# Kernel tuning notes

Hardware: AMD Instinct MI355X
Metric: run time of the kernel (lower is better)

## Reference

```python
import jax, jax.numpy as jnp
import numpy as np

TOP_K = 2
SCALE = 1.0  # score_scale_factor

def setup_inputs() -> dict:
    key = jax.random.key(0)
    ks = jax.random.split(key, 8)
    T, D, E, F = 4096, 1024, 8, 4096
    return {
        "hidden_states": jax.random.normal(ks[0], (T, D), jnp.float32),
        "gw1": jax.random.normal(ks[1], (D, D // 4), jnp.float32) * 0.02,
        "gb1": jnp.zeros((D // 4,), jnp.float32),
        "gw2": jax.random.normal(ks[2], (D // 4, D // 16), jnp.float32) * 0.02,
        "gb2": jnp.zeros((D // 16,), jnp.float32),
        "gw3": jax.random.normal(ks[3], (D // 16, E), jnp.float32) * 0.02,
        "w1": jax.random.normal(ks[4], (E, D, F), jnp.float32) * 0.02,
        "b1": jnp.zeros((E, F), jnp.float32),
        "w2": jax.random.normal(ks[5], (E, F, D), jnp.float32) * 0.02,
        "b2": jnp.zeros((E, D), jnp.float32),
    }

def reference(hidden_states, gw1, gb1, gw2, gb2, gw3, w1, b1, w2, b2):
    h = hidden_states                              # [T, D]
    g = jax.nn.relu(h @ gw1 + gb1)
    g = jax.nn.relu(g @ gw2 + gb2)
    router_logits = g @ gw3                        # [T, E]
    probs = jax.nn.softmax(router_logits.astype(jnp.float32), axis=-1)
    top_w, top_i = jax.lax.top_k(probs, TOP_K)     # [T, k]
    top_w = top_w / jnp.sum(top_w, axis=-1, keepdims=True)
    top_w = top_w.astype(h.dtype)
    T, E = router_logits.shape
    # combine weights: scatter normalized top-k weights into dense [T, E]
    cw = jnp.zeros((T, E), h.dtype).at[jnp.arange(T)[:, None], top_i].add(top_w)
    out = jnp.zeros_like(h)
    for e in range(E):  # small fixed expert count
        y = jax.nn.gelu(h @ w1[e] + b1[e]) @ w2[e] + b2[e]
        out = out + y * (cw[:, e:e + 1] * SCALE)
    return out, router_logits
```

## Files before the change

### kernel.cpp

```cpp
#include <hip/hip_runtime.h>
#include <stdint.h>

#define T_  4096
#define D_  1024
#define E_  8
#define F_  4096
#define H1_ 256
#define H2_ 64
#define SCALE_ 1.0f
#define NROW_ (2 * T_)
#define NT2_ 40

typedef unsigned short ushort_t;
typedef unsigned int   uint32;
typedef __attribute__((ext_vector_type(8))) short  short8;
typedef __attribute__((ext_vector_type(4))) float  f32x4;
typedef __attribute__((ext_vector_type(8))) unsigned short us8;

#define BARRIER() do { asm volatile("" ::: "memory"); __builtin_amdgcn_s_barrier(); asm volatile("" ::: "memory"); } while (0)
#define WAITVM(N) asm volatile("s_waitcnt vmcnt(" #N ")" ::: "memory")

__device__ __forceinline__ ushort_t f2bf(float f) {
  uint32 u = __float_as_uint(f);
  u += 0x7FFFu + ((u >> 16) & 1u);
  return (ushort_t)(u >> 16);
}
__device__ __forceinline__ float gelu_tanh(float x) {
  float u = 0.7978845608028654f * (x + 0.044715f * x * x * x);
  float e = __expf(2.0f * u);
  return 0.5f * x * (1.0f + (1.0f - 2.0f / (e + 1.0f)));
}
__device__ __forceinline__ void gll16(const void* gptr, void* lptr) {
  void* g = const_cast<void*>(gptr);
  __builtin_amdgcn_global_load_lds((__attribute__((address_space(1))) void*)g,
                                   (__attribute__((address_space(3))) void*)lptr,
                                   16, 0, 0);
}

__device__ __forceinline__ void stage8(const ushort_t* a0, const ushort_t* a1,
                                       const ushort_t* b0, const ushort_t* b1,
                                       short8 (*An)[16][64], short8 (*Bn)[16][64], int w) {
  gll16(a0,      &An[0][w * 2 + 0][0]);
  gll16(a0 + 32, &An[1][w * 2 + 0][0]);
  gll16(a1,      &An[0][w * 2 + 1][0]);
  gll16(a1 + 32, &An[1][w * 2 + 1][0]);
  gll16(b0,      &Bn[0][w * 2 + 0][0]);
  gll16(b0 + 32, &Bn[1][w * 2 + 0][0]);
  gll16(b1,      &Bn[0][w * 2 + 1][0]);
  gll16(b1 + 32, &Bn[1][w * 2 + 1][0]);
}

__device__ __forceinline__ void mfma_step64(const short8 (*Ac)[16][64], const short8 (*Bc)[16][64],
                                            int wr, int wc, int lane, f32x4 acc[8][4]) {
#pragma unroll
  for (int ks = 0; ks < 2; ++ks) {
    short8 af[8], bf4[4];
#pragma unroll
    for (int i = 0; i < 8; ++i) af[i] = Ac[ks][wr * 8 + i][lane];
#pragma unroll
    for (int j = 0; j < 4; ++j) bf4[j] = Bc[ks][wc * 4 + j][lane];
#pragma unroll
    for (int i = 0; i < 8; ++i)
#pragma unroll
      for (int j = 0; j < 4; ++j)
        acc[i][j] = __builtin_amdgcn_mfma_f32_16x16x32_bf16(af[i], bf4[j], acc[i][j], 0, 0, 0);
  }
}

__global__ void k_cvt_h(const float* __restrict__ h, ushort_t* __restrict__ hb) {
  int i = (blockIdx.x * 256 + threadIdx.x) * 8;
  float4 a = *(const float4*)(h + i);
  float4 b = *(const float4*)(h + i + 4);
  short8 v;
  v[0] = (short)f2bf(a.x); v[1] = (short)f2bf(a.y);
  v[2] = (short)f2bf(a.z); v[3] = (short)f2bf(a.w);
  v[4] = (short)f2bf(b.x); v[5] = (short)f2bf(b.y);
  v[6] = (short)f2bf(b.z); v[7] = (short)f2bf(b.w);
  *(short8*)(hb + i) = v;
}

__global__ void k_transpose_bf16(const float* __restrict__ in, ushort_t* __restrict__ out,
                                 int R, int C) {
  __shared__ float ltf[64][65];
  const size_t per = (size_t)R * C;
  const float* src = in + per * blockIdx.z;
  ushort_t* dst = out + per * blockIdx.z;
  int r0 = blockIdx.x * 64, c0 = blockIdx.y * 64;
  int tid = threadIdx.x;
  int cg = (tid & 15) * 4;
  int rr = tid >> 4;
#pragma unroll
  for (int rb = 0; rb < 64; rb += 16) {
    int r = rb + rr;
    float4 v = *(const float4*)(src + (size_t)(r0 + r) * C + c0 + cg);
    ltf[r][cg + 0] = v.x; ltf[r][cg + 1] = v.y;
    ltf[r][cg + 2] = v.z; ltf[r][cg + 3] = v.w;
  }
  __syncthreads();
  int c = tid >> 2, rch = (tid & 3) * 16;
  ushort_t tmp[16];
#pragma unroll
  for (int i = 0; i < 16; ++i) tmp[i] = f2bf(ltf[rch + i][c]);
  ushort_t* dp = dst + (size_t)(c0 + c) * R + r0 + rch;
  *(us8*)dp = *(const us8*)&tmp[0];
  *(us8*)(dp + 8) = *(const us8*)&tmp[8];
}

__global__ void k_router1(const float* __restrict__ h, const float* __restrict__ gw1,
                          double* __restrict__ p1) {
  __shared__ float sA[16][65];
  __shared__ float sB[16][65];
  int tx = threadIdx.x, ty = threadIdx.y;
  int tid = ty * 16 + tx;
  int m0 = blockIdx.y * 64, n0 = blockIdx.x * 64;
  int kc = blockIdx.z;
  double acc[4][4] = {};
  for (int k0 = kc * 256; k0 < kc * 256 + 256; k0 += 16) {
    {
      int m = tid & 63, kq = tid >> 6;
      float4 v = *(const float4*)(h + (size_t)(m0 + m) * D_ + k0 + kq * 4);
      sA[kq*4+0][m] = v.x; sA[kq*4+1][m] = v.y; sA[kq*4+2][m] = v.z; sA[kq*4+3][m] = v.w;
    }
    {
      int k = tid >> 4, nq = tid & 15;
      float4 v = *(const float4*)(gw1 + (size_t)(k0 + k) * H1_ + n0 + nq * 4);
      sB[k][nq*4+0] = v.x; sB[k][nq*4+1] = v.y; sB[k][nq*4+2] = v.z; sB[k][nq*4+3] = v.w;
    }
    __syncthreads();
#pragma unroll
    for (int k = 0; k < 16; ++k) {
      float a[4], b[4];
#pragma unroll
      for (int i = 0; i < 4; ++i) a[i] = sA[k][ty + i * 16];
#pragma unroll
      for (int j = 0; j < 4; ++j) b[j] = sB[k][tx * 4 + j];
#pragma unroll
      for (int i = 0; i < 4; ++i)
#pragma unroll
        for (int j = 0; j < 4; ++j)
          acc[i][j] += (double)a[i] * (double)b[j];
    }
    __syncthreads();
  }
  double* pd = p1 + (size_t)kc * T_ * H1_;
  for (int i = 0; i < 4; ++i)
    for (int j = 0; j < 4; ++j) {
      int m = m0 + ty + i * 16, n = n0 + tx * 4 + j;
      pd[(size_t)m * H1_ + n] = acc[i][j];
    }
}

__global__ void k_router23(const double* __restrict__ p1, const float* __restrict__ gb1,
                           const float* __restrict__ gw2, const float* __restrict__ gb2,
                           const float* __restrict__ gw3,
                           float* __restrict__ logits_out, int* __restrict__ tokExp,
                           float* __restrict__ tokW, int* __restrict__ counts) {
  __shared__ double sG1[4][256];
  __shared__ double sG2[4][64];
  __shared__ double sL[4][8];
  int lane = threadIdx.x & 63, wv = threadIdx.x >> 6;
  int t = blockIdx.x * 4 + wv;
  const size_t TH = (size_t)T_ * H1_;
  const double* gp = p1 + (size_t)t * H1_ + lane * 4;
  double s0 = 0, s1 = 0, s2 = 0, s3 = 0;
#pragma unroll
  for (int kc = 0; kc < 4; ++kc) {
    double2 va = *(const double2*)(gp + kc * TH);
    double2 vb = *(const double2*)(gp + kc * TH + 2);
    s0 += va.x; s1 += va.y; s2 += vb.x; s3 += vb.y;
  }
  int hbase = lane * 4;
  s0 += (double)gb1[hbase + 0]; s1 += (double)gb1[hbase + 1];
  s2 += (double)gb1[hbase + 2]; s3 += (double)gb1[hbase + 3];
  sG1[wv][hbase + 0] = s0 > 0.0 ? s0 : 0.0;
  sG1[wv][hbase + 1] = s1 > 0.0 ? s1 : 0.0;
  sG1[wv][hbase + 2] = s2 > 0.0 ? s2 : 0.0;
  sG1[wv][hbase + 3] = s3 > 0.0 ? s3 : 0.0;
  __syncthreads();
  double acc = (double)gb2[lane];
  for (int k = 0; k < H1_; ++k)
    acc += sG1[wv][k] * (double)gw2[k * H2_ + lane];
  sG2[wv][lane] = acc > 0.0 ? acc : 0.0;
  __syncthreads();
  if (lane < 8) {
    double l = 0.0;
    for (int j = 0; j < H2_; ++j) l += sG2[wv][j] * (double)gw3[j * E_ + lane];
    sL[wv][lane] = l;
    logits_out[(size_t)t * E_ + lane] = (float)l;
  }
  __syncthreads();
  if (lane == 0) {
    double best = -1e300, second = -1e300; int bi = 0, si = 0;
    for (int e = 0; e < E_; ++e) {
      double l = sL[wv][e];
      if (l > best)        { second = best; si = bi; best = l; bi = e; }
      else if (l > second) { second = l; si = e; }
    }
    double w0 = 1.0 / (1.0 + exp(second - best));
    tokExp[t*2]   = bi; tokExp[t*2+1] = si;
    tokW[t*2]     = (float)w0;
    tokW[t*2+1]   = (float)(1.0 - w0);
    atomicAdd(&counts[bi], 1);
    atomicAdd(&counts[si], 1);
  }
}

__global__ void k_assign(const int* __restrict__ tokExp, const int* __restrict__ counts,
                         int* cursor, int* __restrict__ list, int* __restrict__ rowOf,
                         int* __restrict__ tileTab) {
  int offs[E_];
  int s = 0;
#pragma unroll
  for (int e = 0; e < E_; ++e) { offs[e] = s; s += counts[e]; }
  if (blockIdx.x == 0 && threadIdx.x == 0) {
    int nt = 0;
    for (int e = 0; e < E_; ++e) {
      int cnt = counts[e];
      for (int m = 0; m * 256 < cnt; ++m) {
        tileTab[nt*3+0] = e;
        tileTab[nt*3+1] = offs[e] + m * 256;
        tileTab[nt*3+2] = (cnt - m * 256) < 256 ? (cnt - m * 256) : 256;
        ++nt;
      }
    }
    for (; nt < NT2_; ++nt) tileTab[nt*3+0] = -1;
  }
  int t = blockIdx.x * 256 + threadIdx.x;
  for (int k = 0; k < 2; ++k) {
    int e = tokExp[t*2+k];
    int pos = atomicAdd(&cursor[e], 1);
    int row = offs[e] + pos;
    list[row] = t;
    rowOf[t*2+k] = row;
  }
}

__global__ __launch_bounds__(512, 1) void k_moe_ffn1(
    const ushort_t* __restrict__ hb, const ushort_t* __restrict__ w1t,
    const float* __restrict__ b1, ushort_t* __restrict__ act,
    const int* __restrict__ list, const int* __restrict__ tileTab) {
  int ti = blockIdx.y;
  int e = tileTab[ti*3+0];
  if (e < 0) return;
  int rowStart = tileTab[ti*3+1];
  int cntTile  = tileTab[ti*3+2];
  int nBase = blockIdx.x * 256;
  const ushort_t* B = w1t + (size_t)e * F_ * D_;
  int tid = threadIdx.x, w = tid >> 6, lane = tid & 63;
  int m16 = lane & 15, kq = lane >> 4;
  __shared__ short8 lA[2][2][16][64];
  __shared__ short8 lB[2][2][16][64];
  int gr0 = rowStart + w * 32 + m16;
  int gr1 = gr0 + 16;
  int t0 = list[min(gr0, NROW_ - 1)];
  int t1 = list[min(gr1, NROW_ - 1)];
  const ushort_t* aS0 = hb + (size_t)t0 * D_ + kq * 8;
  const ushort_t* aS1 = hb + (size_t)t1 * D_ + kq * 8;
  const ushort_t* bS0 = B + (size_t)(nBase + w * 32 + m16) * D_ + kq * 8;
  const ushort_t* bS1 = bS0 + (size_t)16 * D_;
  int wr = w >> 2, wc = w & 3;
  f32x4 acc[8][4] = {};
  stage8(aS0, aS1, bS0, bS1, lA[0], lB[0], w);
  const int NSTEP = D_ / 64;
  for (int t = 0; t < NSTEP - 1; ++t) {
    int k0 = (t + 1) * 64;
    stage8(aS0 + k0, aS1 + k0, bS0 + k0, bS1 + k0, lA[(t + 1) & 1], lB[(t + 1) & 1], w);
    WAITVM(8);
    BARRIER();
    mfma_step64(lA[t & 1], lB[t & 1], wr, wc, lane, acc);
    BARRIER();
  }
  WAITVM(0);
  BARRIER();
  mfma_step64(lA[(NSTEP - 1) & 1], lB[(NSTEP - 1) & 1], wr, wc, lane, acc);
  const float* b1e = b1 + (size_t)e * F_;
  int quad = lane >> 4, cn = lane & 15;
  float bj[4];
#pragma unroll
  for (int j = 0; j < 4; ++j) bj[j] = b1e[nBase + wc * 64 + j * 16 + cn];
#pragma unroll
  for (int i = 0; i < 8; ++i) {
    int lrow = wr * 128 + i * 16 + quad * 4;
#pragma unroll
    for (int r = 0; r < 4; ++r) {
      if (lrow + r < cntTile) {
        size_t gr = (size_t)rowStart + lrow + r;
#pragma unroll
        for (int j = 0; j < 4; ++j) {
          int n = nBase + wc * 64 + j * 16 + cn;
          float x = acc[i][j][r] + bj[j];
          act[gr * F_ + n] = f2bf(gelu_tanh(x));
        }
      }
    }
  }
}

__global__ __launch_bounds__(512, 1) void k_moe_ffn2(
    const ushort_t* __restrict__ act, const ushort_t* __restrict__ w2t,
    float* __restrict__ part, const int* __restrict__ tileTab) {
  int ti = blockIdx.y;
  int e = tileTab[ti*3+0];
  if (e < 0) return;
  int rowStart = tileTab[ti*3+1];
  int cntTile  = tileTab[ti*3+2];
  int kc = blockIdx.z;
  int nBase = blockIdx.x * 256;
  const ushort_t* Bw = w2t + (size_t)e * D_ * F_;
  int tid = threadIdx.x, w = tid >> 6, lane = tid & 63;
  int m16 = lane & 15, kq = lane >> 4;
  __shared__ short8 lA[2][2][16][64];
  __shared__ short8 lB[2][2][16][64];
  int gr0 = rowStart + w * 32 + m16;
  int gr1 = gr0 + 16;
  int kBase = kc * (F_ / 2);
  const ushort_t* aS0 = act + (size_t)min(gr0, NROW_ - 1) * F_ + kBase + kq * 8;
  const ushort_t* aS1 = act + (size_t)min(gr1, NROW_ - 1) * F_ + kBase + kq * 8;
  const ushort_t* bS0 = Bw + (size_t)(nBase + w * 32 + m16) * F_ + kBase + kq * 8;
  const ushort_t* bS1 = bS0 + (size_t)16 * F_;
  int wr = w >> 2, wc = w & 3;
  f32x4 acc[8][4] = {};
  stage8(aS0, aS1, bS0, bS1, lA[0], lB[0], w);
  const int NSTEP = (F_ / 2) / 64;
  for (int t = 0; t < NSTEP - 1; ++t) {
    int k0 = (t + 1) * 64;
    stage8(aS0 + k0, aS1 + k0, bS0 + k0, bS1 + k0, lA[(t + 1) & 1], lB[(t + 1) & 1], w);
    WAITVM(8);
    BARRIER();
    mfma_step64(lA[t & 1], lB[t & 1], wr, wc, lane, acc);
    BARRIER();
  }
  WAITVM(0);
  BARRIER();
  mfma_step64(lA[(NSTEP - 1) & 1], lB[(NSTEP - 1) & 1], wr, wc, lane, acc);
  float* pd = part + (size_t)kc * NROW_ * D_;
  int quad = lane >> 4, cn = lane & 15;
#pragma unroll
  for (int i = 0; i < 8; ++i) {
    int lrow = wr * 128 + i * 16 + quad * 4;
#pragma unroll
    for (int r = 0; r < 4; ++r) {
      if (lrow + r < cntTile) {
        size_t gr = (size_t)rowStart + lrow + r;
#pragma unroll
        for (int j = 0; j < 4; ++j) {
          int n = nBase + wc * 64 + j * 16 + cn;
          pd[gr * D_ + n] = acc[i][j][r];
        }
      }
    }
  }
}

__global__ void k_combine(const float* __restrict__ part, const int* __restrict__ rowOf,
                          const int* __restrict__ tokExp, const float* __restrict__ tokW,
                          const float* __restrict__ b2, float* __restrict__ out) {
  int t = blockIdx.x;
  int rA = rowOf[t*2], rB = rowOf[t*2+1];
  int eA = tokExp[t*2], eB = tokExp[t*2+1];
  float wA = tokW[t*2] * SCALE_, wB = tokW[t*2+1] * SCALE_;
  int d = threadIdx.x * 4;
  const size_t P = (size_t)NROW_ * D_;
  float4 a0 = *(const float4*)(part + (size_t)rA * D_ + d);
  float4 a1 = *(const float4*)(part + P + (size_t)rA * D_ + d);
  float4 b0 = *(const float4*)(part + (size_t)rB * D_ + d);
  float4 b1 = *(const float4*)(part + P + (size_t)rB * D_ + d);
  float4 ba = *(const float4*)(b2 + (size_t)eA * D_ + d);
  float4 bb = *(const float4*)(b2 + (size_t)eB * D_ + d);
  float4 o;
  o.x = wA * (a0.x + a1.x + ba.x) + wB * (b0.x + b1.x + bb.x);
  o.y = wA * (a0.y + a1.y + ba.y) + wB * (b0.y + b1.y + bb.y);
  o.z = wA * (a0.z + a1.z + ba.z) + wB * (b0.z + b1.z + bb.z);
  o.w = wA * (a0.w + a1.w + ba.w) + wB * (b0.w + b1.w + bb.w);
  *(float4*)(out + (size_t)t * D_ + d) = o;
}

extern "C" void kernel_launch(void* const* d_in, const int* in_sizes, int n_in,
                              void* d_out, int out_size, void* d_ws, size_t ws_size,
                              hipStream_t stream) {
  const float* h   = (const float*)d_in[0];
  const float* gw1 = (const float*)d_in[1];
  const float* gb1 = (const float*)d_in[2];
  const float* gw2 = (const float*)d_in[3];
  const float* gb2 = (const float*)d_in[4];
  const float* gw3 = (const float*)d_in[5];
  const float* w1  = (const float*)d_in[6];
  const float* b1  = (const float*)d_in[7];
  const float* w2  = (const float*)d_in[8];
  const float* b2  = (const float*)d_in[9];
  float* out    = (float*)d_out;
  float* logits = out + (size_t)T_ * D_;

  char* ws = (char*)d_ws;
  size_t o = 0;
  auto alloc = [&](size_t bytes) -> void* {
    o = (o + 255) & ~(size_t)255;
    void* p = ws + o;
    o += bytes;
    return p;
  };
  int*      counts  = (int*)alloc(2 * E_ * 4);
  int*      cursor  = counts + E_;
  int*      tileTab = (int*)alloc((size_t)NT2_ * 3 * 4);
  int*      tokExp  = (int*)alloc((size_t)T_ * 2 * 4);
  float*    tokW    = (float*)alloc((size_t)T_ * 2 * 4);
  int*      list    = (int*)alloc((size_t)NROW_ * 4);
  int*      rowOf   = (int*)alloc((size_t)NROW_ * 4);
  ushort_t* hb      = (ushort_t*)alloc((size_t)T_ * D_ * 2);
  ushort_t* w2t     = (ushort_t*)alloc((size_t)E_ * D_ * F_ * 2);
  char*     bigA    = (char*)alloc((size_t)NROW_ * F_ * 2);
  double*   p1      = (double*)bigA;
  ushort_t* act     = (ushort_t*)bigA;
  char*     bigB    = (char*)alloc((size_t)E_ * D_ * F_ * 2);
  ushort_t* w1t     = (ushort_t*)bigB;
  float*    part    = (float*)bigB;
  (void)ws_size; (void)in_sizes; (void)n_in; (void)out_size;

  hipMemsetAsync(counts, 0, 2 * E_ * 4, stream);
  k_cvt_h<<<T_ * D_ / 2048, 256, 0, stream>>>(h, hb);
  k_transpose_bf16<<<dim3(D_ / 64, F_ / 64, E_), 256, 0, stream>>>(w1, w1t, D_, F_);
  k_transpose_bf16<<<dim3(F_ / 64, D_ / 64, E_), 256, 0, stream>>>(w2, w2t, F_, D_);
  k_router1<<<dim3(H1_ / 64, T_ / 64, 4), dim3(16, 16), 0, stream>>>(h, gw1, p1);
  k_router23<<<T_ / 4, 256, 0, stream>>>(p1, gb1, gw2, gb2, gw3, logits, tokExp, tokW, counts);
  k_assign<<<T_ / 256, 256, 0, stream>>>(tokExp, counts, cursor, list, rowOf, tileTab);
  k_moe_ffn1<<<dim3(F_ / 256, NT2_), 512, 0, stream>>>(hb, w1t, b1, act, list, tileTab);
  k_moe_ffn2<<<dim3(D_ / 256, NT2_, 2), 512, 0, stream>>>(act, w2t, part, tileTab);
  k_combine<<<T_, 256, 0, stream>>>(part, rowOf, tokExp, tokW, b2, out);
}
```

Baseline: 914.5 us.

## Use persistent atomic work queues for expert FFN GEMMs and widen split-K

Both expert GEMM kernels become persistent: 256 blocks pull (tile, column-block[, k-chunk]) items from an atomic counter instead of launching one block per tile, so blocks for empty tile slots no longer occupy the grid and load balances across CUs. The second GEMM can split K four ways when the workspace has room, giving more work items per tile. The combine kernel then sums a variable number of partials. This trades extra partial-sum traffic and per-item atomic and barrier overhead for better CU utilization.

```diff
diff --git a/kernel.cpp b/kernel.cpp
--- a/kernel.cpp
+++ b/kernel.cpp
@@ -238,140 +238,162 @@
 __global__ __launch_bounds__(512, 1) void k_moe_ffn1(
     const ushort_t* __restrict__ hb, const ushort_t* __restrict__ w1t,
     const float* __restrict__ b1, ushort_t* __restrict__ act,
-    const int* __restrict__ list, const int* __restrict__ tileTab) {
-  int ti = blockIdx.y;
-  int e = tileTab[ti*3+0];
-  if (e < 0) return;
-  int rowStart = tileTab[ti*3+1];
-  int cntTile  = tileTab[ti*3+2];
-  int nBase = blockIdx.x * 256;
-  const ushort_t* B = w1t + (size_t)e * F_ * D_;
+    const int* __restrict__ list, const int* __restrict__ tileTab, int* q) {
+  __shared__ short8 lA[2][2][16][64];
+  __shared__ short8 lB[2][2][16][64];
+  __shared__ int sIdx;
   int tid = threadIdx.x, w = tid >> 6, lane = tid & 63;
   int m16 = lane & 15, kq = lane >> 4;
+  int wr = w >> 2, wc = w & 3;
+  int quad = lane >> 4, cn = lane & 15;
+  for (;;) {
+    __syncthreads();
+    if (tid == 0) sIdx = atomicAdd(q, 1);
+    __syncthreads();
+    int idx = sIdx;
+    if (idx >= NT2_ * 16) return;
+    int ti = idx >> 4, nb = idx & 15;
+    int e = tileTab[ti*3+0];
+    if (e < 0) continue;
+    int rowStart = tileTab[ti*3+1];
+    int cntTile  = tileTab[ti*3+2];
+    int nBase = nb * 256;
+    const ushort_t* B = w1t + (size_t)e * F_ * D_;
+    int gr0 = rowStart + w * 32 + m16;
+    int gr1 = gr0 + 16;
+    int t0 = list[min(gr0, NROW_ - 1)];
+    int t1 = list[min(gr1, NROW_ - 1)];
+    const ushort_t* aS0 = hb + (size_t)t0 * D_ + kq * 8;
+    const ushort_t* aS1 = hb + (size_t)t1 * D_ + kq * 8;
+    const ushort_t* bS0 = B + (size_t)(nBase + w * 32 + m16) * D_ + kq * 8;
+    const ushort_t* bS1 = bS0 + (size_t)16 * D_;
+    f32x4 acc[8][4] = {};
+    stage8(aS0, aS1, bS0, bS1, lA[0], lB[0], w);
+    const int NSTEP = D_ / 64;
+    for (int t = 0; t < NSTEP - 1; ++t) {
+      int k0 = (t + 1) * 64;
+      stage8(aS0 + k0, aS1 + k0, bS0 + k0, bS1 + k0, lA[(t + 1) & 1], lB[(t + 1) & 1], w);
+      WAITVM(8);
+      BARRIER();
+      mfma_step64(lA[t & 1], lB[t & 1], wr, wc, lane, acc);
+      BARRIER();
+    }
+    WAITVM(0);
+    BARRIER();
+    mfma_step64(lA[(NSTEP - 1) & 1], lB[(NSTEP - 1) & 1], wr, wc, lane, acc);
+    const float* b1e = b1 + (size_t)e * F_;
+    float bj[4];
+#pragma unroll
+    for (int j = 0; j < 4; ++j) bj[j] = b1e[nBase + wc * 64 + j * 16 + cn];
+#pragma unroll
+    for (int i = 0; i < 8; ++i) {
+      int lrow = wr * 128 + i * 16 + quad * 4;
+#pragma unroll
+      for (int r = 0; r < 4; ++r) {
+        if (lrow + r < cntTile) {
+          size_t gr = (size_t)rowStart + lrow + r;
+#pragma unroll
+          for (int j = 0; j < 4; ++j) {
+            int n = nBase + wc * 64 + j * 16 + cn;
+            float x = acc[i][j][r] + bj[j];
+            act[gr * F_ + n] = f2bf(gelu_tanh(x));
+          }
+        }
+      }
+    }
+  }
+}
+
+__global__ __launch_bounds__(512, 1) void k_moe_ffn2(
+    const ushort_t* __restrict__ act, const ushort_t* __restrict__ w2t,
+    float* __restrict__ part, const int* __restrict__ tileTab, int* q, int KC) {
   __shared__ short8 lA[2][2][16][64];
   __shared__ short8 lB[2][2][16][64];
-  int gr0 = rowStart + w * 32 + m16;
-  int gr1 = gr0 + 16;
-  int t0 = list[min(gr0, NROW_ - 1)];
-  int t1 = list[min(gr1, NROW_ - 1)];
-  const ushort_t* aS0 = hb + (size_t)t0 * D_ + kq * 8;
-  const ushort_t* aS1 = hb + (size_t)t1 * D_ + kq * 8;
-  const ushort_t* bS0 = B + (size_t)(nBase + w * 32 + m16) * D_ + kq * 8;
-  const ushort_t* bS1 = bS0 + (size_t)16 * D_;
+  __shared__ int sIdx;
+  int tid = threadIdx.x, w = tid >> 6, lane = tid & 63;
+  int m16 = lane & 15, kq = lane >> 4;
   int wr = w >> 2, wc = w & 3;
-  f32x4 acc[8][4] = {};
-  stage8(aS0, aS1, bS0, bS1, lA[0], lB[0], w);
-  const int NSTEP = D_ / 64;
-  for (int t = 0; t < NSTEP - 1; ++t) {
-    int k0 = (t + 1) * 64;
-    stage8(aS0 + k0, aS1 + k0, bS0 + k0, bS1 + k0, lA[(t + 1) & 1], lB[(t + 1) & 1], w);
-    WAITVM(8);
+  int quad = lane >> 4, cn = lane & 15;
+  const int ipt = 4 * KC;
+  const int kcs = F_ / KC;
+  const int NSTEP = kcs / 64;
+  for (;;) {
+    __syncthreads();
+    if (tid == 0) sIdx = atomicAdd(q, 1);
+    __syncthreads();
+    int idx = sIdx;
+    if (idx >= NT2_ * ipt) return;
+    int ti = idx / ipt, sub = idx - ti * ipt;
+    int nb = sub / KC, kc = sub - nb * KC;
+    int e = tileTab[ti*3+0];
+    if (e < 0) continue;
+    int rowStart = tileTab[ti*3+1];
+    int cntTile  = tileTab[ti*3+2];
+    int nBase = nb * 256;
+    int kBase = kc * kcs;
+    const ushort_t* Bw = w2t + (size_t)e * D_ * F_;
+    int gr0 = rowStart + w * 32 + m16;
+    int gr1 = gr0 + 16;
+    const ushort_t* aS0 = act + (size_t)min(gr0, NROW_ - 1) * F_ + kBase + kq * 8;
+    const ushort_t* aS1 = act + (size_t)min(gr1, NROW_ - 1) * F_ + kBase + kq * 8;
+    const ushort_t* bS0 = Bw + (size_t)(nBase + w * 32 + m16) * F_ + kBase + kq * 8;
+    const ushort_t* bS1 = bS0 + (size_t)16 * F_;
+    f32x4 acc[8][4] = {};
+    stage8(aS0, aS1, bS0, bS1, lA[0], lB[0], w);
+    for (int t = 0; t < NSTEP - 1; ++t) {
+      int k0 = (t + 1) * 64;
+      stage8(aS0 + k0, aS1 + k0, bS0 + k0, bS1 + k0, lA[(t + 1) & 1], lB[(t + 1) & 1], w);
+      WAITVM(8);
+      BARRIER();
+      mfma_step64(lA[t & 1], lB[t & 1], wr, wc, lane, acc);
+      BARRIER();
+    }
+    WAITVM(0);
     BARRIER();
-    mfma_step64(lA[t & 1], lB[t & 1], wr, wc, lane, acc);
-    BARRIER();
-  }
-  WAITVM(0);
-  BARRIER();
-  mfma_step64(lA[(NSTEP - 1) & 1], lB[(NSTEP - 1) & 1], wr, wc, lane, acc);
-  const float* b1e = b1 + (size_t)e * F_;
-  int quad = lane >> 4, cn = lane & 15;
-  float bj[4];
-#pragma unroll
-  for (int j = 0; j < 4; ++j) bj[j] = b1e[nBase + wc * 64 + j * 16 + cn];
-#pragma unroll
-  for (int i = 0; i < 8; ++i) {
-    int lrow = wr * 128 + i * 16 + quad * 4;
-#pragma unroll
-    for (int r = 0; r < 4; ++r) {
-      if (lrow + r < cntTile) {
-        size_t gr = (size_t)rowStart + lrow + r;
-#pragma unroll
-        for (int j = 0; j < 4; ++j) {
-          int n = nBase + wc * 64 + j * 16 + cn;
-          float x = acc[i][j][r] + bj[j];
-          act[gr * F_ + n] = f2bf(gelu_tanh(x));
+    mfma_step64(lA[(NSTEP - 1) & 1], lB[(NSTEP - 1) & 1], wr, wc, lane, acc);
+    float* pd = part + (size_t)kc * NROW_ * D_;
+#pragma unroll
+    for (int i = 0; i < 8; ++i) {
+      int lrow = wr * 128 + i * 16 + quad * 4;
+#pragma unroll
+      for (int r = 0; r < 4; ++r) {
+        if (lrow + r < cntTile) {
+          size_t gr = (size_t)rowStart + lrow + r;
+#pragma unroll
+          for (int j = 0; j < 4; ++j) {
+            int n = nBase + wc * 64 + j * 16 + cn;
+            pd[gr * D_ + n] = acc[i][j][r];
+          }
         }
       }
     }
   }
 }
 
-__global__ __launch_bounds__(512, 1) void k_moe_ffn2(
-    const ushort_t* __restrict__ act, const ushort_t* __restrict__ w2t,
-    float* __restrict__ part, const int* __restrict__ tileTab) {
-  int ti = blockIdx.y;
-  int e = tileTab[ti*3+0];
-  if (e < 0) return;
-  int rowStart = tileTab[ti*3+1];
-  int cntTile  = tileTab[ti*3+2];
-  int kc = blockIdx.z;
-  int nBase = blockIdx.x * 256;
-  const ushort_t* Bw = w2t + (size_t)e * D_ * F_;
-  int tid = threadIdx.x, w = tid >> 6, lane = tid & 63;
-  int m16 = lane & 15, kq = lane >> 4;
-  __shared__ short8 lA[2][2][16][64];
-  __shared__ short8 lB[2][2][16][64];
-  int gr0 = rowStart + w * 32 + m16;
-  int gr1 = gr0 + 16;
-  int kBase = kc * (F_ / 2);
-  const ushort_t* aS0 = act + (size_t)min(gr0, NROW_ - 1) * F_ + kBase + kq * 8;
-  const ushort_t* aS1 = act + (size_t)min(gr1, NROW_ - 1) * F_ + kBase + kq * 8;
-  const ushort_t* bS0 = Bw + (size_t)(nBase + w * 32 + m16) * F_ + kBase + kq * 8;
-  const ushort_t* bS1 = bS0 + (size_t)16 * F_;
-  int wr = w >> 2, wc = w & 3;
-  f32x4 acc[8][4] = {};
-  stage8(aS0, aS1, bS0, bS1, lA[0], lB[0], w);
-  const int NSTEP = (F_ / 2) / 64;
-  for (int t = 0; t < NSTEP - 1; ++t) {
-    int k0 = (t + 1) * 64;
-    stage8(aS0 + k0, aS1 + k0, bS0 + k0, bS1 + k0, lA[(t + 1) & 1], lB[(t + 1) & 1], w);
-    WAITVM(8);
-    BARRIER();
-    mfma_step64(lA[t & 1], lB[t & 1], wr, wc, lane, acc);
-    BARRIER();
-  }
-  WAITVM(0);
-  BARRIER();
-  mfma_step64(lA[(NSTEP - 1) & 1], lB[(NSTEP - 1) & 1], wr, wc, lane, acc);
-  float* pd = part + (size_t)kc * NROW_ * D_;
-  int quad = lane >> 4, cn = lane & 15;
-#pragma unroll
-  for (int i = 0; i < 8; ++i) {
-    int lrow = wr * 128 + i * 16 + quad * 4;
-#pragma unroll
-    for (int r = 0; r < 4; ++r) {
-      if (lrow + r < cntTile) {
-        size_t gr = (size_t)rowStart + lrow + r;
-#pragma unroll
-        for (int j = 0; j < 4; ++j) {
-          int n = nBase + wc * 64 + j * 16 + cn;
-          pd[gr * D_ + n] = acc[i][j][r];
-        }
-      }
-    }
-  }
-}
-
 __global__ void k_combine(const float* __restrict__ part, const int* __restrict__ rowOf,
                           const int* __restrict__ tokExp, const float* __restrict__ tokW,
-                          const float* __restrict__ b2, float* __restrict__ out) {
+                          const float* __restrict__ b2, float* __restrict__ out, int KC) {
   int t = blockIdx.x;
   int rA = rowOf[t*2], rB = rowOf[t*2+1];
   int eA = tokExp[t*2], eB = tokExp[t*2+1];
   float wA = tokW[t*2] * SCALE_, wB = tokW[t*2+1] * SCALE_;
   int d = threadIdx.x * 4;
   const size_t P = (size_t)NROW_ * D_;
-  float4 a0 = *(const float4*)(part + (size_t)rA * D_ + d);
-  float4 a1 = *(const float4*)(part + P + (size_t)rA * D_ + d);
-  float4 b0 = *(const float4*)(part + (size_t)rB * D_ + d);
-  float4 b1 = *(const float4*)(part + P + (size_t)rB * D_ + d);
+  float sax = 0, say = 0, saz = 0, saw = 0;
+  float sbx = 0, sby = 0, sbz = 0, sbw = 0;
+  for (int k = 0; k < KC; ++k) {
+    float4 a = *(const float4*)(part + (size_t)k * P + (size_t)rA * D_ + d);
+    float4 b = *(const float4*)(part + (size_t)k * P + (size_t)rB * D_ + d);
+    sax += a.x; say += a.y; saz += a.z; saw += a.w;
+    sbx += b.x; sby += b.y; sbz += b.z; sbw += b.w;
+  }
   float4 ba = *(const float4*)(b2 + (size_t)eA * D_ + d);
   float4 bb = *(const float4*)(b2 + (size_t)eB * D_ + d);
   float4 o;
-  o.x = wA * (a0.x + a1.x + ba.x) + wB * (b0.x + b1.x + bb.x);
-  o.y = wA * (a0.y + a1.y + ba.y) + wB * (b0.y + b1.y + bb.y);
-  o.z = wA * (a0.z + a1.z + ba.z) + wB * (b0.z + b1.z + bb.z);
-  o.w = wA * (a0.w + a1.w + ba.w) + wB * (b0.w + b1.w + bb.w);
+  o.x = wA * (sax + ba.x) + wB * (sbx + bb.x);
+  o.y = wA * (say + ba.y) + wB * (sby + bb.y);
+  o.z = wA * (saz + ba.z) + wB * (sbz + bb.z);
+  o.w = wA * (saw + ba.w) + wB * (sbw + bb.w);
   *(float4*)(out + (size_t)t * D_ + d) = o;
 }
 
@@ -399,8 +421,9 @@
     o += bytes;
     return p;
   };
-  int*      counts  = (int*)alloc(2 * E_ * 4);
+  int*      counts  = (int*)alloc((2 * E_ + 2) * 4);
   int*      cursor  = counts + E_;
+  int*      qq      = counts + 2 * E_;
   int*      tileTab = (int*)alloc((size_t)NT2_ * 3 * 4);
   int*      tokExp  = (int*)alloc((size_t)T_ * 2 * 4);
   float*    tokW    = (float*)alloc((size_t)T_ * 2 * 4);
@@ -411,19 +434,23 @@
   char*     bigA    = (char*)alloc((size_t)NROW_ * F_ * 2);
   double*   p1      = (double*)bigA;
   ushort_t* act     = (ushort_t*)bigA;
-  char*     bigB    = (char*)alloc((size_t)E_ * D_ * F_ * 2);
+  size_t oAligned = (o + 255) & ~(size_t)255;
+  size_t w1tBytes = (size_t)E_ * D_ * F_ * 2;
+  int KC = (ws_size >= oAligned + (size_t)4 * NROW_ * D_ * 4) ? 4 : 2;
+  size_t partBytes = (size_t)KC * NROW_ * D_ * 4;
+  char*     bigB    = (char*)alloc(partBytes > w1tBytes ? partBytes : w1tBytes);
   ushort_t* w1t     = (ushort_t*)bigB;
   float*    part    = (float*)bigB;
-  (void)ws_size; (void)in_sizes; (void)n_in; (void)out_size;
-
-  hipMemsetAsync(counts, 0, 2 * E_ * 4, stream);
+  (void)in_sizes; (void)n_in; (void)out_size;
+
+  hipMemsetAsync(counts, 0, (2 * E_ + 2) * 4, stream);
   k_cvt_h<<<T_ * D_ / 2048, 256, 0, stream>>>(h, hb);
   k_transpose_bf16<<<dim3(D_ / 64, F_ / 64, E_), 256, 0, stream>>>(w1, w1t, D_, F_);
   k_transpose_bf16<<<dim3(F_ / 64, D_ / 64, E_), 256, 0, stream>>>(w2, w2t, F_, D_);
   k_router1<<<dim3(H1_ / 64, T_ / 64, 4), dim3(16, 16), 0, stream>>>(h, gw1, p1);
   k_router23<<<T_ / 4, 256, 0, stream>>>(p1, gb1, gw2, gb2, gw3, logits, tokExp, tokW, counts);
   k_assign<<<T_ / 256, 256, 0, stream>>>(tokExp, counts, cursor, list, rowOf, tileTab);
-  k_moe_ffn1<<<dim3(F_ / 256, NT2_), 512, 0, stream>>>(hb, w1t, b1, act, list, tileTab);
-  k_moe_ffn2<<<dim3(D_ / 256, NT2_, 2), 512, 0, stream>>>(act, w2t, part, tileTab);
-  k_combine<<<T_, 256, 0, stream>>>(part, rowOf, tokExp, tokW, b2, out);
-}
+  k_moe_ffn1<<<256, 512, 0, stream>>>(hb, w1t, b1, act, list, tileTab, qq + 0);
+  k_moe_ffn2<<<256, 512, 0, stream>>>(act, w2t, part, tileTab, qq + 1, KC);
+  k_combine<<<T_, 256, 0, stream>>>(part, rowOf, tokExp, tokW, b2, out, KC);
+}
```

New measurement: 906.9 us. About the same (-0.8%).
